# Performance work log

Measured on AMD Instinct MI355X. Metric: run time of the kernel, lower is better.

## Reference

```python
import jax, jax.numpy as jnp
import numpy as np

HIDDEN = [256, 256, 256]
COND = 30
NB_STEPS = 20  # Clenshaw-Curtis quadrature order -> NB_STEPS+1 nodes


def cc_weights_steps(nb_steps):
    # Clenshaw-Curtis weights/nodes on [-1, 1] (UMNN compute_cc_weights)
    lam = np.arange(nb_steps + 1, dtype=np.float64).reshape(-1, 1)
    lam = np.cos(lam @ lam.T * np.pi / nb_steps)
    lam[:, 0] *= 0.5
    lam[:, -1] *= 0.5
    lam = lam * 2.0 / nb_steps
    W = np.arange(nb_steps + 1, dtype=np.float64).reshape(-1, 1)
    W[1::2] = 0.0
    W = 2.0 / (1.0 - W ** 2)
    W[0] = 1.0
    W[1::2] = 0.0
    cc_w = (lam.T @ W).flatten()          # [S]
    steps = np.cos(np.arange(nb_steps + 1) * np.pi / nb_steps)  # [S]
    return jnp.asarray(cc_w, jnp.float32), jnp.asarray(steps, jnp.float32)


def mlp(inp, Ws, bs):
    # IntegrandNet: Linear+ReLU chain, final layer ELU(x)+1 (strictly positive)
    y = inp
    n = len(Ws)
    for i in range(n):
        y = y @ Ws[i] + bs[i]
        y = jax.nn.relu(y) if i < n - 1 else jax.nn.elu(y) + 1.0
    return y[..., 0]


def setup_inputs() -> dict:
    key = jax.random.key(0)
    ks = jax.random.split(key, 12)
    B, D = 512, 32
    x = jax.random.normal(ks[0], (B, D), jnp.float32)
    h = jax.random.normal(ks[1], (B, D, COND), jnp.float32)
    dims = [1 + COND] + HIDDEN + [1]
    params = {}
    for i in range(len(dims) - 1):
        params[f"W{i}"] = jax.random.normal(ks[2 + 2 * i], (dims[i], dims[i + 1]), jnp.float32) / np.sqrt(dims[i]).astype(np.float32)
        params[f"b{i}"] = jnp.zeros((dims[i + 1],), jnp.float32)
    return {"x": x, "h": h, **params}


def reference(x, h, W0, b0, W1, b1, W2, b2, W3, b3):
    Ws = [W0, W1, W2, W3]
    bs = [b0, b1, b2, b3]
    B, D = x.shape
    S = NB_STEPS + 1
    cc_w, steps = cc_weights_steps(NB_STEPS)
    # x0 = 0, xT = x -> quadrature nodes X = xT * (steps + 1) / 2, shape [B, S, D]
    X = x[:, None, :] * (steps[None, :, None] + 1.0) * 0.5
    hb = jnp.broadcast_to(h[:, None, :, :], (B, S, D, COND))
    inp = jnp.concatenate([X[..., None], hb], axis=-1)  # [B, S, D, 1+COND]
    f = mlp(inp, Ws, bs)                                 # [B, S, D] positive integrand
    z_est = jnp.einsum('bsd,s->bd', f, cc_w) * x * 0.5   # integral over [0, x]
    z = z_est + h[:, :, 0]                               # add offset z0
    # second output: integrand evaluated at x (the transform's Jacobian diag)
    inp_x = jnp.concatenate([x[..., None], h], axis=-1)  # [B, D, 1+COND]
    jac = mlp(inp_x, Ws, bs)                             # [B, D]
    return z, jac
```

## Files before the change

kernel.cpp:

```cpp
#include <hip/hip_runtime.h>
#include <math.h>

#define NB        512
#define ND        32
#define NCOND     30
#define NS        21
#define NBD       (NB*ND)
#define NROWS     (NBD*NS)
#define MBLK      128
#define NBLOCKS   (NROWS/MBLK)

#define W0P_ELEMS (1*16*64*8)
#define W1P_ELEMS (8*16*64*8)
#define W3P_ELEMS (8*64*8)
#define WP_TOTAL  (W0P_ELEMS + 2*W1P_ELEMS + W3P_ELEMS)

typedef __bf16 bf8 __attribute__((ext_vector_type(8)));
typedef float  fx4 __attribute__((ext_vector_type(4)));
typedef unsigned short us8 __attribute__((ext_vector_type(8)));

__device__ __forceinline__ unsigned short f2bf(float f) {
  unsigned int u = __float_as_uint(f);
  u += 0x7FFFu + ((u >> 16) & 1u);
  return (unsigned short)(u >> 16);
}

__global__ void prep_pack(const float* __restrict__ W0,
                          const float* __restrict__ W1,
                          const float* __restrict__ W2,
                          const float* __restrict__ W3,
                          unsigned short* __restrict__ wp) {
  int t = blockIdx.x * blockDim.x + threadIdx.x;
  if (t >= WP_TOTAL / 8) return;
  int base = t * 8;
  us8 out;
  if (base >= W0P_ELEMS + 2 * W1P_ELEMS) {
    int rem  = base - (W0P_ELEMS + 2 * W1P_ELEMS);
    int lane = (rem >> 3) & 63;
    int ktl  = rem >> 9;
    int k0   = ktl * 32 + (lane >> 4) * 8;
#pragma unroll
    for (int i = 0; i < 8; ++i)
      out[i] = ((lane & 15) == 0) ? f2bf(W3[k0 + i]) : (unsigned short)0;
  } else {
    const float* W; int rem, K;
    if (base < W0P_ELEMS)                  { W = W0; rem = base;                 K = 31;  }
    else if (base < W0P_ELEMS + W1P_ELEMS) { W = W1; rem = base - W0P_ELEMS;     K = 256; }
    else                                   { W = W2; rem = base - W0P_ELEMS - W1P_ELEMS; K = 256; }
    int lane = (rem >> 3) & 63;
    int ct   = (rem >> 9) & 15;
    int ktl  =  rem >> 13;
    int j  = ct * 16 + (lane & 15);
    int k0 = ktl * 32 + (lane >> 4) * 8;
#pragma unroll
    for (int i = 0; i < 8; ++i) {
      int k = k0 + i;
      out[i] = (k < K) ? f2bf(W[k * 256 + j]) : (unsigned short)0;
    }
  }
  *reinterpret_cast<us8*>(wp + base) = out;
}


#define DENSE256(WBASE)                                                          \
  {                                                                              \
    _Pragma("unroll")                                                            \
    for (int rt = 0; rt < 4; ++rt)                                               \
      _Pragma("unroll")                                                          \
      for (int ct = 0; ct < 4; ++ct) acc[rt][ct] = fx4{0.f, 0.f, 0.f, 0.f};      \
    _Pragma("unroll")                                                            \
    for (int kt = 0; kt < 8; ++kt) {                                             \
      bf8 w0 = *reinterpret_cast<const bf8*>((WBASE) + ((kt * 16 + cgrp * 4 + 0) * 64 + lane) * 8); \
      bf8 w1 = *reinterpret_cast<const bf8*>((WBASE) + ((kt * 16 + cgrp * 4 + 1) * 64 + lane) * 8); \
      bf8 w2 = *reinterpret_cast<const bf8*>((WBASE) + ((kt * 16 + cgrp * 4 + 2) * 64 + lane) * 8); \
      bf8 w3 = *reinterpret_cast<const bf8*>((WBASE) + ((kt * 16 + cgrp * 4 + 3) * 64 + lane) * 8); \
      _Pragma("unroll")                                                          \
      for (int rt = 0; rt < 4; ++rt) {                                           \
        int m = rgrp * 64 + rt * 16 + colb;                                      \
        unsigned int off = ((unsigned int)(m * 512 + kt * 64 + khalf * 16))      \
                         ^ ((unsigned int)((m & 15) << 4));                      \
        bf8 a = *reinterpret_cast<const bf8*>(ldsAct + off);                     \
        acc[rt][0] = __builtin_amdgcn_mfma_f32_16x16x32_bf16(w0, a, acc[rt][0], 0, 0, 0); \
        acc[rt][1] = __builtin_amdgcn_mfma_f32_16x16x32_bf16(w1, a, acc[rt][1], 0, 0, 0); \
        acc[rt][2] = __builtin_amdgcn_mfma_f32_16x16x32_bf16(w2, a, acc[rt][2], 0, 0, 0); \
        acc[rt][3] = __builtin_amdgcn_mfma_f32_16x16x32_bf16(w3, a, acc[rt][3], 0, 0, 0); \
      }                                                                          \
    }                                                                            \
  }

#define ACT_STORE(BIAS)                                                          \
  {                                                                              \
    float4 bv0 = *reinterpret_cast<const float4*>((BIAS) + (cgrp * 4 + 0) * 16 + khalf * 4); \
    float4 bv1 = *reinterpret_cast<const float4*>((BIAS) + (cgrp * 4 + 1) * 16 + khalf * 4); \
    float4 bv2 = *reinterpret_cast<const float4*>((BIAS) + (cgrp * 4 + 2) * 16 + khalf * 4); \
    float4 bv3 = *reinterpret_cast<const float4*>((BIAS) + (cgrp * 4 + 3) * 16 + khalf * 4); \
    _Pragma("unroll")                                                            \
    for (int rt = 0; rt < 4; ++rt) {                                             \
      int m = rgrp * 64 + rt * 16 + colb;                                        \
      unsigned int sbase = (unsigned int)(m * 512);                              \
      unsigned int swz   = (unsigned int)((m & 15) << 4);                        \
      _Pragma("unroll")                                                          \
      for (int ct = 0; ct < 4; ++ct) {                                           \
        float4 bv = (ct == 0) ? bv0 : (ct == 1) ? bv1 : (ct == 2) ? bv2 : bv3;   \
        int n0 = (cgrp * 4 + ct) * 16 + khalf * 4;                               \
        float v0 = fmaxf(acc[rt][ct][0] + bv.x, 0.f);                            \
        float v1 = fmaxf(acc[rt][ct][1] + bv.y, 0.f);                            \
        float v2 = fmaxf(acc[rt][ct][2] + bv.z, 0.f);                            \
        float v3 = fmaxf(acc[rt][ct][3] + bv.w, 0.f);                            \
        unsigned int p0, p1;                                                     \
        asm("v_cvt_pk_bf16_f32 %0, %1, %2" : "=v"(p0) : "v"(v0), "v"(v1));       \
        asm("v_cvt_pk_bf16_f32 %0, %1, %2" : "=v"(p1) : "v"(v2), "v"(v3));       \
        uint2 pk; pk.x = p0; pk.y = p1;                                          \
        *reinterpret_cast<uint2*>(ldsAct + ((sbase + (unsigned int)(n0 * 2)) ^ swz)) = pk; \
      }                                                                          \
    }                                                                            \
  }

__global__ __launch_bounds__(512, 2)
void mlp_kernel(const float* __restrict__ x, const float* __restrict__ h,
                const float* __restrict__ b0, const float* __restrict__ b1,
                const float* __restrict__ b2, const float* __restrict__ b3,
                const unsigned short* __restrict__ wp,
                float* __restrict__ fbuf) {
  __shared__ __align__(16) unsigned char ldsAct[128 * 512];
  __shared__ __align__(16) unsigned char ldsIn[128 * 64];

  int tid  = threadIdx.x;
  int wv   = tid >> 6;
  int lane = tid & 63;
  int rgrp = wv >> 2;
  int cgrp = wv & 3;
  int colb  = lane & 15;
  int khalf = lane >> 4;
  int R0 = blockIdx.x * MBLK;

  {
    int r = tid >> 2;
    int q = tid & 3;
    int gr = R0 + r;
    unsigned int bd = (unsigned int)gr / NS;
    int s = gr - (int)bd * NS;
    float xv = x[bd];
    float node = xv * (cosf((float)s * 0.15707963267948966f) + 1.0f) * 0.5f;
    const float* hrow = h + bd * NCOND;
    us8 au;
#pragma unroll
    for (int i = 0; i < 8; ++i) {
      int c = q * 8 + i;
      float v;
      if (c == 0)       v = node;
      else if (c <= 30) v = hrow[c - 1];
      else              v = 0.0f;
      au[i] = f2bf(v);
    }
    unsigned int off = (unsigned int)(r * 64 + q * 16) ^ (unsigned int)((r & 3) << 4);
    *reinterpret_cast<us8*>(ldsIn + off) = au;
  }
  __syncthreads();

  fx4 acc[4][4];

  {
#pragma unroll
    for (int rt = 0; rt < 4; ++rt)
#pragma unroll
      for (int ct = 0; ct < 4; ++ct) acc[rt][ct] = fx4{0.f, 0.f, 0.f, 0.f};
    bf8 w0 = *reinterpret_cast<const bf8*>(wp + ((cgrp * 4 + 0) * 64 + lane) * 8);
    bf8 w1 = *reinterpret_cast<const bf8*>(wp + ((cgrp * 4 + 1) * 64 + lane) * 8);
    bf8 w2 = *reinterpret_cast<const bf8*>(wp + ((cgrp * 4 + 2) * 64 + lane) * 8);
    bf8 w3 = *reinterpret_cast<const bf8*>(wp + ((cgrp * 4 + 3) * 64 + lane) * 8);
#pragma unroll
    for (int rt = 0; rt < 4; ++rt) {
      int m = rgrp * 64 + rt * 16 + colb;
      unsigned int off = (unsigned int)(m * 64 + khalf * 16) ^ (unsigned int)((m & 3) << 4);
      bf8 a = *reinterpret_cast<const bf8*>(ldsIn + off);
      acc[rt][0] = __builtin_amdgcn_mfma_f32_16x16x32_bf16(w0, a, acc[rt][0], 0, 0, 0);
      acc[rt][1] = __builtin_amdgcn_mfma_f32_16x16x32_bf16(w1, a, acc[rt][1], 0, 0, 0);
      acc[rt][2] = __builtin_amdgcn_mfma_f32_16x16x32_bf16(w2, a, acc[rt][2], 0, 0, 0);
      acc[rt][3] = __builtin_amdgcn_mfma_f32_16x16x32_bf16(w3, a, acc[rt][3], 0, 0, 0);
    }
    ACT_STORE(b0);
  }
  __syncthreads();

  const unsigned short* wb1 = wp + W0P_ELEMS;
  const unsigned short* wb2 = wp + W0P_ELEMS + W1P_ELEMS;
  const unsigned short* w3p = wp + W0P_ELEMS + 2 * W1P_ELEMS;

  DENSE256(wb1);
  __syncthreads();
  ACT_STORE(b1);
  __syncthreads();

  DENSE256(wb2);
  __syncthreads();
  ACT_STORE(b2);
  __syncthreads();

  if (cgrp == 0) {
    fx4 a30 = fx4{0.f, 0.f, 0.f, 0.f};
    fx4 a31 = fx4{0.f, 0.f, 0.f, 0.f};
    fx4 a32 = fx4{0.f, 0.f, 0.f, 0.f};
    fx4 a33 = fx4{0.f, 0.f, 0.f, 0.f};
#pragma unroll
    for (int kt = 0; kt < 8; ++kt) {
      bf8 w3f = *reinterpret_cast<const bf8*>(w3p + (kt * 64 + lane) * 8);
#pragma unroll
      for (int rt = 0; rt < 4; ++rt) {
        int m = rgrp * 64 + rt * 16 + colb;
        unsigned int off = ((unsigned int)(m * 512 + kt * 64 + khalf * 16))
                         ^ ((unsigned int)((m & 15) << 4));
        bf8 a = *reinterpret_cast<const bf8*>(ldsAct + off);
        if      (rt == 0) a30 = __builtin_amdgcn_mfma_f32_16x16x32_bf16(w3f, a, a30, 0, 0, 0);
        else if (rt == 1) a31 = __builtin_amdgcn_mfma_f32_16x16x32_bf16(w3f, a, a31, 0, 0, 0);
        else if (rt == 2) a32 = __builtin_amdgcn_mfma_f32_16x16x32_bf16(w3f, a, a32, 0, 0, 0);
        else              a33 = __builtin_amdgcn_mfma_f32_16x16x32_bf16(w3f, a, a33, 0, 0, 0);
      }
    }
    if (lane < 16) {
      float bias3 = b3[0];
#pragma unroll
      for (int rt = 0; rt < 4; ++rt) {
        float y = ((rt == 0) ? a30[0] : (rt == 1) ? a31[0] : (rt == 2) ? a32[0] : a33[0]) + bias3;
        float f = (y > 0.f) ? (y + 1.f) : expf(y);
        fbuf[R0 + rgrp * 64 + rt * 16 + lane] = f;
      }
    }
  }
}

__global__ void reduce_kernel(const float* __restrict__ x, const float* __restrict__ h,
                              const float* __restrict__ fbuf, float* __restrict__ out) {
  __shared__ float ccw[NS];
  int tid = threadIdx.x;
  if (tid < NS) {
    double acc = 0.0;
#pragma unroll
    for (int i = 0; i <= 20; i += 2) {
      double wi = (i == 0) ? 1.0 : 2.0 / (1.0 - (double)(i * i));
      acc += cos((double)(i * tid) * 3.141592653589793 / 20.0) * wi;
    }
    double edge = (tid == 0 || tid == 20) ? 0.5 : 1.0;
    ccw[tid] = (float)(acc * 0.1 * edge);
  }
  __syncthreads();
  int t = blockIdx.x * blockDim.x + tid;
  if (t >= NBD) return;
  const float* fb = fbuf + t * NS;
  float acc = 0.f;
#pragma unroll
  for (int i = 0; i < NS; ++i) acc += fb[i] * ccw[i];
  float z = acc * x[t] * 0.5f + h[t * NCOND];
  out[t] = z;
  out[NBD + t] = fb[0];
}

extern "C" void kernel_launch(void* const* d_in, const int* in_sizes, int n_in,
                              void* d_out, int out_size, void* d_ws, size_t ws_size,
                              hipStream_t stream) {
  (void)in_sizes; (void)n_in; (void)out_size; (void)ws_size;
  const float* x  = (const float*)d_in[0];
  const float* h  = (const float*)d_in[1];
  const float* W0 = (const float*)d_in[2];
  const float* b0 = (const float*)d_in[3];
  const float* W1 = (const float*)d_in[4];
  const float* b1 = (const float*)d_in[5];
  const float* W2 = (const float*)d_in[6];
  const float* b2 = (const float*)d_in[7];
  const float* W3 = (const float*)d_in[8];
  const float* b3 = (const float*)d_in[9];

  unsigned short* wp = (unsigned short*)d_ws;
  float* fbuf = (float*)((char*)d_ws + WP_TOTAL * sizeof(unsigned short));
  float* out  = (float*)d_out;

  prep_pack<<<(WP_TOTAL / 8 + 255) / 256, 256, 0, stream>>>(W0, W1, W2, W3, wp);
  mlp_kernel<<<NBLOCKS, 512, 0, stream>>>(x, h, b0, b1, b2, b3, wp, fbuf);
  reduce_kernel<<<(NBD + 255) / 256, 256, 0, stream>>>(x, h, fbuf, out);
}
```

Measured before the change: 123.7 us.

## Software-pipeline weight loads across k-steps and layers with double-buffered registers

Each dense layer's k-loop is rewritten so weight fragments for step k+2 are fetched from global memory while step k's MFMAs run, using two register sets. The first fragments of the next layer are prefetched before the barrier, and the first layer's weights are loaded before input staging. MFMA bursts are wrapped in s_setprio, and launch bounds drop to one block per SM so the extra registers fit. The aim is to hide global/L2 weight-load latency behind matrix math, at the cost of lower occupancy and more register pressure.

```diff
diff --git a/kernel.cpp b/kernel.cpp
--- a/kernel.cpp
+++ b/kernel.cpp
@@ -62,31 +62,67 @@
 }
 
 
-#define DENSE256(WBASE)                                                          \
+#define ACC_ZERO                                                                 \
+  _Pragma("unroll")                                                              \
+  for (int rt = 0; rt < 4; ++rt)                                                 \
+    _Pragma("unroll")                                                            \
+    for (int ct = 0; ct < 4; ++ct) acc[rt][ct] = fx4{0.f, 0.f, 0.f, 0.f};
+
+#define LOADW4(S0,S1,S2,S3, WB, KT)                                              \
+  S0 = *reinterpret_cast<const bf8*>((WB) + (((KT) * 16 + cgrp * 4 + 0) * 64 + lane) * 8); \
+  S1 = *reinterpret_cast<const bf8*>((WB) + (((KT) * 16 + cgrp * 4 + 1) * 64 + lane) * 8); \
+  S2 = *reinterpret_cast<const bf8*>((WB) + (((KT) * 16 + cgrp * 4 + 2) * 64 + lane) * 8); \
+  S3 = *reinterpret_cast<const bf8*>((WB) + (((KT) * 16 + cgrp * 4 + 3) * 64 + lane) * 8);
+
+#define KSTEP(W0_,W1_,W2_,W3_, KT)                                               \
   {                                                                              \
-    _Pragma("unroll")                                                            \
-    for (int rt = 0; rt < 4; ++rt)                                               \
-      _Pragma("unroll")                                                          \
-      for (int ct = 0; ct < 4; ++ct) acc[rt][ct] = fx4{0.f, 0.f, 0.f, 0.f};      \
-    _Pragma("unroll")                                                            \
-    for (int kt = 0; kt < 8; ++kt) {                                             \
-      bf8 w0 = *reinterpret_cast<const bf8*>((WBASE) + ((kt * 16 + cgrp * 4 + 0) * 64 + lane) * 8); \
-      bf8 w1 = *reinterpret_cast<const bf8*>((WBASE) + ((kt * 16 + cgrp * 4 + 1) * 64 + lane) * 8); \
-      bf8 w2 = *reinterpret_cast<const bf8*>((WBASE) + ((kt * 16 + cgrp * 4 + 2) * 64 + lane) * 8); \
-      bf8 w3 = *reinterpret_cast<const bf8*>((WBASE) + ((kt * 16 + cgrp * 4 + 3) * 64 + lane) * 8); \
-      _Pragma("unroll")                                                          \
-      for (int rt = 0; rt < 4; ++rt) {                                           \
-        int m = rgrp * 64 + rt * 16 + colb;                                      \
-        unsigned int off = ((unsigned int)(m * 512 + kt * 64 + khalf * 16))      \
-                         ^ ((unsigned int)((m & 15) << 4));                      \
-        bf8 a = *reinterpret_cast<const bf8*>(ldsAct + off);                     \
-        acc[rt][0] = __builtin_amdgcn_mfma_f32_16x16x32_bf16(w0, a, acc[rt][0], 0, 0, 0); \
-        acc[rt][1] = __builtin_amdgcn_mfma_f32_16x16x32_bf16(w1, a, acc[rt][1], 0, 0, 0); \
-        acc[rt][2] = __builtin_amdgcn_mfma_f32_16x16x32_bf16(w2, a, acc[rt][2], 0, 0, 0); \
-        acc[rt][3] = __builtin_amdgcn_mfma_f32_16x16x32_bf16(w3, a, acc[rt][3], 0, 0, 0); \
-      }                                                                          \
-    }                                                                            \
-  }
+    int m0 = rgrp * 64 +  0 + colb;                                              \
+    int m1 = rgrp * 64 + 16 + colb;                                              \
+    int m2 = rgrp * 64 + 32 + colb;                                              \
+    int m3 = rgrp * 64 + 48 + colb;                                              \
+    bf8 a0 = *reinterpret_cast<const bf8*>(ldsAct + (((unsigned)(m0 * 512 + (KT) * 64 + khalf * 16)) ^ ((unsigned)((m0 & 15) << 4)))); \
+    bf8 a1 = *reinterpret_cast<const bf8*>(ldsAct + (((unsigned)(m1 * 512 + (KT) * 64 + khalf * 16)) ^ ((unsigned)((m1 & 15) << 4)))); \
+    bf8 a2 = *reinterpret_cast<const bf8*>(ldsAct + (((unsigned)(m2 * 512 + (KT) * 64 + khalf * 16)) ^ ((unsigned)((m2 & 15) << 4)))); \
+    bf8 a3 = *reinterpret_cast<const bf8*>(ldsAct + (((unsigned)(m3 * 512 + (KT) * 64 + khalf * 16)) ^ ((unsigned)((m3 & 15) << 4)))); \
+    __builtin_amdgcn_s_setprio(1);                                               \
+    acc[0][0] = __builtin_amdgcn_mfma_f32_16x16x32_bf16(W0_, a0, acc[0][0], 0, 0, 0); \
+    acc[0][1] = __builtin_amdgcn_mfma_f32_16x16x32_bf16(W1_, a0, acc[0][1], 0, 0, 0); \
+    acc[0][2] = __builtin_amdgcn_mfma_f32_16x16x32_bf16(W2_, a0, acc[0][2], 0, 0, 0); \
+    acc[0][3] = __builtin_amdgcn_mfma_f32_16x16x32_bf16(W3_, a0, acc[0][3], 0, 0, 0); \
+    acc[1][0] = __builtin_amdgcn_mfma_f32_16x16x32_bf16(W0_, a1, acc[1][0], 0, 0, 0); \
+    acc[1][1] = __builtin_amdgcn_mfma_f32_16x16x32_bf16(W1_, a1, acc[1][1], 0, 0, 0); \
+    acc[1][2] = __builtin_amdgcn_mfma_f32_16x16x32_bf16(W2_, a1, acc[1][2], 0, 0, 0); \
+    acc[1][3] = __builtin_amdgcn_mfma_f32_16x16x32_bf16(W3_, a1, acc[1][3], 0, 0, 0); \
+    acc[2][0] = __builtin_amdgcn_mfma_f32_16x16x32_bf16(W0_, a2, acc[2][0], 0, 0, 0); \
+    acc[2][1] = __builtin_amdgcn_mfma_f32_16x16x32_bf16(W1_, a2, acc[2][1], 0, 0, 0); \
+    acc[2][2] = __builtin_amdgcn_mfma_f32_16x16x32_bf16(W2_, a2, acc[2][2], 0, 0, 0); \
+    acc[2][3] = __builtin_amdgcn_mfma_f32_16x16x32_bf16(W3_, a2, acc[2][3], 0, 0, 0); \
+    acc[3][0] = __builtin_amdgcn_mfma_f32_16x16x32_bf16(W0_, a3, acc[3][0], 0, 0, 0); \
+    acc[3][1] = __builtin_amdgcn_mfma_f32_16x16x32_bf16(W1_, a3, acc[3][1], 0, 0, 0); \
+    acc[3][2] = __builtin_amdgcn_mfma_f32_16x16x32_bf16(W2_, a3, acc[3][2], 0, 0, 0); \
+    acc[3][3] = __builtin_amdgcn_mfma_f32_16x16x32_bf16(W3_, a3, acc[3][3], 0, 0, 0); \
+    __builtin_amdgcn_s_setprio(0);                                               \
+  }
+
+#define DENSE_PIPE(WB, NWB)                                                      \
+  KSTEP(wa0,wa1,wa2,wa3, 0) LOADW4(wa0,wa1,wa2,wa3, WB, 2)                       \
+  KSTEP(wb0,wb1,wb2,wb3, 1) LOADW4(wb0,wb1,wb2,wb3, WB, 3)                       \
+  KSTEP(wa0,wa1,wa2,wa3, 2) LOADW4(wa0,wa1,wa2,wa3, WB, 4)                       \
+  KSTEP(wb0,wb1,wb2,wb3, 3) LOADW4(wb0,wb1,wb2,wb3, WB, 5)                       \
+  KSTEP(wa0,wa1,wa2,wa3, 4) LOADW4(wa0,wa1,wa2,wa3, WB, 6)                       \
+  KSTEP(wb0,wb1,wb2,wb3, 5) LOADW4(wb0,wb1,wb2,wb3, WB, 7)                       \
+  KSTEP(wa0,wa1,wa2,wa3, 6) LOADW4(wa0,wa1,wa2,wa3, NWB, 0)                      \
+  KSTEP(wb0,wb1,wb2,wb3, 7) LOADW4(wb0,wb1,wb2,wb3, NWB, 1)
+
+#define DENSE_LAST(WB)                                                           \
+  KSTEP(wa0,wa1,wa2,wa3, 0) LOADW4(wa0,wa1,wa2,wa3, WB, 2)                       \
+  KSTEP(wb0,wb1,wb2,wb3, 1) LOADW4(wb0,wb1,wb2,wb3, WB, 3)                       \
+  KSTEP(wa0,wa1,wa2,wa3, 2) LOADW4(wa0,wa1,wa2,wa3, WB, 4)                       \
+  KSTEP(wb0,wb1,wb2,wb3, 3) LOADW4(wb0,wb1,wb2,wb3, WB, 5)                       \
+  KSTEP(wa0,wa1,wa2,wa3, 4) LOADW4(wa0,wa1,wa2,wa3, WB, 6)                       \
+  KSTEP(wb0,wb1,wb2,wb3, 5) LOADW4(wb0,wb1,wb2,wb3, WB, 7)                       \
+  KSTEP(wa0,wa1,wa2,wa3, 6)                                                      \
+  KSTEP(wb0,wb1,wb2,wb3, 7)
 
 #define ACT_STORE(BIAS)                                                          \
   {                                                                              \
@@ -116,7 +152,7 @@
     }                                                                            \
   }
 
-__global__ __launch_bounds__(512, 2)
+__global__ __launch_bounds__(512, 1)
 void mlp_kernel(const float* __restrict__ x, const float* __restrict__ h,
                 const float* __restrict__ b0, const float* __restrict__ b1,
                 const float* __restrict__ b2, const float* __restrict__ b3,
@@ -133,6 +169,13 @@
   int colb  = lane & 15;
   int khalf = lane >> 4;
   int R0 = blockIdx.x * MBLK;
+
+  const unsigned short* wb1p = wp + W0P_ELEMS;
+  const unsigned short* wb2p = wp + W0P_ELEMS + W1P_ELEMS;
+  const unsigned short* w3p  = wp + W0P_ELEMS + 2 * W1P_ELEMS;
+
+  bf8 wa0, wa1, wa2, wa3, wb0, wb1, wb2, wb3;
+  LOADW4(wa0, wa1, wa2, wa3, wp, 0);
 
   {
     int r = tid >> 2;
@@ -161,38 +204,31 @@
   fx4 acc[4][4];
 
   {
-#pragma unroll
-    for (int rt = 0; rt < 4; ++rt)
-#pragma unroll
-      for (int ct = 0; ct < 4; ++ct) acc[rt][ct] = fx4{0.f, 0.f, 0.f, 0.f};
-    bf8 w0 = *reinterpret_cast<const bf8*>(wp + ((cgrp * 4 + 0) * 64 + lane) * 8);
-    bf8 w1 = *reinterpret_cast<const bf8*>(wp + ((cgrp * 4 + 1) * 64 + lane) * 8);
-    bf8 w2 = *reinterpret_cast<const bf8*>(wp + ((cgrp * 4 + 2) * 64 + lane) * 8);
-    bf8 w3 = *reinterpret_cast<const bf8*>(wp + ((cgrp * 4 + 3) * 64 + lane) * 8);
+    ACC_ZERO;
 #pragma unroll
     for (int rt = 0; rt < 4; ++rt) {
       int m = rgrp * 64 + rt * 16 + colb;
       unsigned int off = (unsigned int)(m * 64 + khalf * 16) ^ (unsigned int)((m & 3) << 4);
       bf8 a = *reinterpret_cast<const bf8*>(ldsIn + off);
-      acc[rt][0] = __builtin_amdgcn_mfma_f32_16x16x32_bf16(w0, a, acc[rt][0], 0, 0, 0);
-      acc[rt][1] = __builtin_amdgcn_mfma_f32_16x16x32_bf16(w1, a, acc[rt][1], 0, 0, 0);
-      acc[rt][2] = __builtin_amdgcn_mfma_f32_16x16x32_bf16(w2, a, acc[rt][2], 0, 0, 0);
-      acc[rt][3] = __builtin_amdgcn_mfma_f32_16x16x32_bf16(w3, a, acc[rt][3], 0, 0, 0);
-    }
+      acc[rt][0] = __builtin_amdgcn_mfma_f32_16x16x32_bf16(wa0, a, acc[rt][0], 0, 0, 0);
+      acc[rt][1] = __builtin_amdgcn_mfma_f32_16x16x32_bf16(wa1, a, acc[rt][1], 0, 0, 0);
+      acc[rt][2] = __builtin_amdgcn_mfma_f32_16x16x32_bf16(wa2, a, acc[rt][2], 0, 0, 0);
+      acc[rt][3] = __builtin_amdgcn_mfma_f32_16x16x32_bf16(wa3, a, acc[rt][3], 0, 0, 0);
+    }
+    LOADW4(wa0, wa1, wa2, wa3, wb1p, 0);
+    LOADW4(wb0, wb1, wb2, wb3, wb1p, 1);
     ACT_STORE(b0);
   }
   __syncthreads();
 
-  const unsigned short* wb1 = wp + W0P_ELEMS;
-  const unsigned short* wb2 = wp + W0P_ELEMS + W1P_ELEMS;
-  const unsigned short* w3p = wp + W0P_ELEMS + 2 * W1P_ELEMS;
-
-  DENSE256(wb1);
+  ACC_ZERO;
+  DENSE_PIPE(wb1p, wb2p);
   __syncthreads();
   ACT_STORE(b1);
   __syncthreads();
 
-  DENSE256(wb2);
+  ACC_ZERO;
+  DENSE_LAST(wb2p);
   __syncthreads();
   ACT_STORE(b2);
   __syncthreads();
```

Result: faster. 118.6 us (-4.1%).
